# Kernel optimization log

Measured on AMD Instinct MI355X. Metric: run time of the kernel, lower is better.

Reference implementation:

```python
import jax, jax.numpy as jnp
import numpy as np

B, S, D, H = 2, 2048, 2048, 16
DH = D // H  # 128


def setup_inputs() -> dict:
    key = jax.random.key(0)
    ks = jax.random.split(key, 7)
    x = jax.random.normal(ks[0], (B, S, D), dtype=jnp.float32)
    # causal mask [b, s, s], True = attend
    mask = jnp.broadcast_to(jnp.tril(jnp.ones((S, S), dtype=bool)), (B, S, S))
    scale = 1.0 / np.sqrt(D)
    Wq = jax.random.normal(ks[1], (D, H, DH), dtype=jnp.float32) * scale
    Wk = jax.random.normal(ks[2], (D, 1, DH), dtype=jnp.float32) * scale
    Wv = jax.random.normal(ks[3], (D, 1, DH), dtype=jnp.float32) * scale
    Wo = jax.random.normal(ks[4], (H, DH, D), dtype=jnp.float32) * scale
    bo = jnp.zeros((D,), dtype=jnp.float32)
    return {"x": x, "mask": mask, "Wq": Wq, "Wk": Wk, "Wv": Wv, "Wo": Wo, "bo": bo}


def reference(x, mask, Wq, Wk, Wv, Wo, bo):
    # projections: q [b,s,h,dh]; k,v [b,s,1,dh] (single shared KV head)
    q = jnp.einsum("bsd,dhe->bshe", x, Wq)
    k = jnp.einsum("bsd,dhe->bshe", x, Wk)[:, :, 0, :]  # [b,s,dh]
    v = jnp.einsum("bsd,dhe->bshe", x, Wv)[:, :, 0, :]  # [b,s,dh]
    # scores [b,h,s,s] with 1/sqrt(d_head) scaling
    scores = jnp.einsum("bqhe,bke->bhqk", q, k) / jnp.sqrt(
        jnp.asarray(q.shape[-1], dtype=q.dtype)
    )
    big_neg = jnp.finfo(scores.dtype).min
    scores = jnp.where(mask[:, None, :, :], scores, big_neg)
    probs = jax.nn.softmax(scores, axis=-1)
    attn = jnp.einsum("bhqk,bke->bhqe", probs, v)  # [b,h,s,dh]
    # output projection contracting (head, d_head) -> d_state, with bias
    out = jnp.einsum("bhqe,hed->bqd", attn, Wo) + bo
    return out
```

## Files before the change

### kernel.cpp

```cpp
#include <hip/hip_runtime.h>
#include <cmath>
#include <cstdint>

typedef __bf16 bf16;
typedef __bf16 bf16x8 __attribute__((ext_vector_type(8)));
typedef __bf16 bf16x4 __attribute__((ext_vector_type(4)));
typedef float f32x4 __attribute__((ext_vector_type(4)));

#define SDIM 2048
#define DDIM 2048
#define NQKV 2304
#define DH   128

__device__ __forceinline__ void glds16(const bf16* g, bf16* l) {
    __builtin_amdgcn_global_load_lds(
        (const __attribute__((address_space(1))) void*)g,
        (__attribute__((address_space(3))) void*)l, 16, 0, 0);
}

#define MEMFENCE() asm volatile("" ::: "memory")
#define SBAR() do { MEMFENCE(); __builtin_amdgcn_s_barrier(); MEMFENCE(); } while (0)

__global__ __launch_bounds__(256) void prep_kernel(const float* __restrict__ x,
                                                   const float* __restrict__ Wq,
                                                   const float* __restrict__ Wk,
                                                   const float* __restrict__ Wv,
                                                   const float* __restrict__ Wo,
                                                   bf16* __restrict__ xb,
                                                   bf16* __restrict__ Wqkv_t,
                                                   bf16* __restrict__ Wo_t) {
    __shared__ float tile[32][33];
    int bx = blockIdx.x;
    if (bx < 8192) {
        int i = bx * 256 + threadIdx.x;
        float4 v = reinterpret_cast<const float4*>(x)[i];
        bf16x4 o;
        o[0] = (bf16)v.x; o[1] = (bf16)v.y; o[2] = (bf16)v.z; o[3] = (bf16)v.w;
        reinterpret_cast<bf16x4*>(xb)[i] = o;
        return;
    }
    bx -= 8192;
    const float* src; bf16* dst; int srcN; int t;
    if (bx < 4096)      { src = Wq; dst = Wqkv_t;                      srcN = 2048; t = bx; }
    else if (bx < 4352) { src = Wk; dst = Wqkv_t + (size_t)2048*2048;  srcN = 128;  t = bx - 4096; }
    else if (bx < 4608) { src = Wv; dst = Wqkv_t + (size_t)2176*2048;  srcN = 128;  t = bx - 4352; }
    else                { src = Wo; dst = Wo_t;                        srcN = 2048; t = bx - 4608; }
    const int srcK = 2048;
    int ntx = srcN >> 5;
    int n0 = (t % ntx) * 32, k0 = (t / ntx) * 32;
    int tx = threadIdx.x & 31;
    int ty = threadIdx.x >> 5;
    for (int i = 0; i < 4; i++)
        tile[ty + i*8][tx] = src[(size_t)(k0 + ty + i*8) * srcN + n0 + tx];
    __syncthreads();
    for (int i = 0; i < 4; i++)
        dst[(size_t)(n0 + ty + i*8) * srcK + k0 + tx] = (bf16)tile[tx][ty + i*8];
}

__global__ __launch_bounds__(256) void vtrans_kernel(const bf16* __restrict__ QKV,
                                                     bf16* __restrict__ Vt) {
    __shared__ bf16 tile[32][33];
    int tx = threadIdx.x & 31;
    int ty = threadIdx.x >> 5;
    int d0 = blockIdx.x * 32;
    int s0 = blockIdx.y * 32;
    int b  = blockIdx.z;
    for (int i = 0; i < 4; i++)
        tile[ty + i*8][tx] = QKV[((size_t)b * SDIM + s0 + ty + i*8) * NQKV + 2176 + d0 + tx];
    __syncthreads();
    for (int i = 0; i < 4; i++)
        Vt[((size_t)b * DH + d0 + ty + i*8) * SDIM + s0 + tx] = tile[tx][ty + i*8];
}

template<int WRITE_F32>
__global__ __launch_bounds__(512, 2) void gemm8_kernel(const bf16* __restrict__ A,
                                                       const bf16* __restrict__ Bt,
                                                       void* __restrict__ Cout,
                                                       const float* __restrict__ bias,
                                                       int N) {
    constexpr int K  = 2048;
    constexpr int NT = 32;
    __shared__ bf16 smem[65536];

    const int tid  = threadIdx.x;
    const int wave = tid >> 6, lane = tid & 63;
    const int quad = lane >> 4, l15 = lane & 15;
    const int wm = wave >> 2, wn = wave & 3;
    const int tm = blockIdx.x * 256, tn = blockIdx.y * 256;

    const int r0 = wave * 32 + (lane >> 2);
    const int cs = (lane & 3) ^ ((lane >> 3) & 3);
    const bf16* Ag = A  + (size_t)(tm + r0) * K + cs * 8;
    const bf16* Bg = Bt + (size_t)(tn + r0) * K + cs * 8;
    bf16* Asl = smem + wave * 1024;
    bf16* Bsl = smem + 32768 + wave * 1024;

    auto STAGE_A = [&](int t, int kh) {
        if (t < NT) {
            const bf16* s = Ag + t * 64 + kh * 32;
            bf16* d = Asl + (t & 1) * 16384 + kh * 8192;
            glds16(s, d);
            glds16(s + 16 * K, d + 512);
        }
    };
    auto STAGE_B = [&](int t, int kh) {
        if (t < NT) {
            const bf16* s = Bg + t * 64 + kh * 32;
            bf16* d = Bsl + (t & 1) * 16384 + kh * 8192;
            glds16(s, d);
            glds16(s + 16 * K, d + 512);
        }
    };

    const int rsw  = (l15 >> 1) & 3;
    const int aoff = (wm * 128 + l15) * 32 + ((quad ^ rsw) * 8);
    const int boff = (wn * 64  + l15) * 32 + ((quad ^ rsw) * 8);

    f32x4 acc[8][4];
#pragma unroll
    for (int m = 0; m < 8; m++)
#pragma unroll
        for (int n = 0; n < 4; n++) acc[m][n] = (f32x4)0.0f;

    STAGE_A(0, 0); STAGE_B(0, 0);
    STAGE_A(0, 1); STAGE_B(0, 1);
    STAGE_A(1, 0); STAGE_B(1, 0);
    asm volatile("s_waitcnt vmcnt(4)" ::: "memory");
    SBAR();

    bf16x8 av[4], bv[4];
    for (int t = 0; t < NT; ++t) {
        const int buf = t & 1;
        const bf16* Sa = smem + buf * 16384;
        const bf16* Sb = smem + 32768 + buf * 16384;

#pragma unroll
        for (int m = 0; m < 4; m++) av[m] = *reinterpret_cast<const bf16x8*>(Sa + aoff + m * 512);
#pragma unroll
        for (int n = 0; n < 4; n++) bv[n] = *reinterpret_cast<const bf16x8*>(Sb + boff + n * 512);
        STAGE_A(t + 1, 1);
        SBAR();
        __builtin_amdgcn_s_setprio(1);
#pragma unroll
        for (int m = 0; m < 4; m++)
#pragma unroll
            for (int n = 0; n < 4; n++)
                acc[m][n] = __builtin_amdgcn_mfma_f32_16x16x32_bf16(av[m], bv[n], acc[m][n], 0, 0, 0);
        __builtin_amdgcn_s_setprio(0);
        SBAR();

#pragma unroll
        for (int m = 0; m < 4; m++) av[m] = *reinterpret_cast<const bf16x8*>(Sa + aoff + 2048 + m * 512);
        STAGE_B(t + 1, 1);
        SBAR();
        __builtin_amdgcn_s_setprio(1);
#pragma unroll
        for (int m = 0; m < 4; m++)
#pragma unroll
            for (int n = 0; n < 4; n++)
                acc[4 + m][n] = __builtin_amdgcn_mfma_f32_16x16x32_bf16(av[m], bv[n], acc[4 + m][n], 0, 0, 0);
        __builtin_amdgcn_s_setprio(0);
        if (t + 1 < NT) { asm volatile("s_waitcnt vmcnt(8)" ::: "memory"); }
        else            { asm volatile("s_waitcnt vmcnt(0)" ::: "memory"); }
        SBAR();

#pragma unroll
        for (int m = 0; m < 4; m++) av[m] = *reinterpret_cast<const bf16x8*>(Sa + 8192 + aoff + m * 512);
#pragma unroll
        for (int n = 0; n < 4; n++) bv[n] = *reinterpret_cast<const bf16x8*>(Sb + 8192 + boff + n * 512);
        STAGE_A(t + 2, 0);
        SBAR();
        __builtin_amdgcn_s_setprio(1);
#pragma unroll
        for (int m = 0; m < 4; m++)
#pragma unroll
            for (int n = 0; n < 4; n++)
                acc[m][n] = __builtin_amdgcn_mfma_f32_16x16x32_bf16(av[m], bv[n], acc[m][n], 0, 0, 0);
        __builtin_amdgcn_s_setprio(0);
        SBAR();

#pragma unroll
        for (int m = 0; m < 4; m++) av[m] = *reinterpret_cast<const bf16x8*>(Sa + 8192 + aoff + 2048 + m * 512);
        STAGE_B(t + 2, 0);
        SBAR();
        __builtin_amdgcn_s_setprio(1);
#pragma unroll
        for (int m = 0; m < 4; m++)
#pragma unroll
            for (int n = 0; n < 4; n++)
                acc[4 + m][n] = __builtin_amdgcn_mfma_f32_16x16x32_bf16(av[m], bv[n], acc[4 + m][n], 0, 0, 0);
        __builtin_amdgcn_s_setprio(0);
        if (t + 2 < NT) { asm volatile("s_waitcnt vmcnt(4)" ::: "memory"); }
        else            { asm volatile("s_waitcnt vmcnt(0)" ::: "memory"); }
        SBAR();
    }

#pragma unroll
    for (int m = 0; m < 8; m++)
#pragma unroll
        for (int n = 0; n < 4; n++)
#pragma unroll
            for (int r = 0; r < 4; r++) {
                int row = tm + wm * 128 + m * 16 + quad * 4 + r;
                int col = tn + wn * 64 + n * 16 + l15;
                float v = acc[m][n][r];
                if (WRITE_F32)
                    reinterpret_cast<float*>(Cout)[(size_t)row * N + col] = v + bias[col];
                else
                    reinterpret_cast<bf16*>(Cout)[(size_t)row * N + col] = (bf16)v;
            }
}

#define FPLD 72

__global__ __launch_bounds__(512) void flash_kernel(const bf16* __restrict__ QKV,
                                                    const bf16* __restrict__ Vt,
                                                    bf16* __restrict__ attn) {
    __shared__ bf16 KVS[16384];
    __shared__ bf16 Ps[8 * 16 * FPLD];
    bf16* Ks  = KVS;
    bf16* Vts = KVS + 8192;

    const int tid  = threadIdx.x;
    const int wave = tid >> 6, lane = tid & 63;
    const int quad = lane >> 4, l15 = lane & 15;
    const int bx = blockIdx.x;
    const int qs = 255 - (bx >> 1);
    const int b  = bx & 1;
    const int q  = qs * 8 + wave;
    const size_t rowbase = (size_t)b * SDIM;
    const bf16* Vtb = Vt + (size_t)b * DH * SDIM;
    const float scale = 0.088388347648318447f;

    const int s0 = wave, s1 = wave + 8;
    const int krow0 = s0*4 + (lane >> 4), krow1 = s1*4 + (lane >> 4);
    const int kchunk = lane & 15;
    const bf16* kg0 = QKV + (rowbase + krow0) * NQKV + 2048 + ((kchunk ^ (krow0 & 15)) * 8);
    const bf16* kg1 = QKV + (rowbase + krow1) * NQKV + 2048 + ((kchunk ^ (krow1 & 15)) * 8);
    bf16* kl0 = Ks + s0 * 512;
    bf16* kl1 = Ks + s1 * 512;
    const int vrow0 = s0*8 + (lane >> 3), vrow1 = s1*8 + (lane >> 3);
    const int vchunk = lane & 7;
    const bf16* vg0 = Vtb + (size_t)vrow0 * SDIM + ((vchunk ^ (vrow0 & 7)) * 8);
    const bf16* vg1 = Vtb + (size_t)vrow1 * SDIM + ((vchunk ^ (vrow1 & 7)) * 8);
    bf16* vl0 = Vts + s0 * 512;
    bf16* vl1 = Vts + s1 * 512;

    bf16x8 qf[4];
    {
        const bf16* qp = QKV + (rowbase + q) * NQKV + l15 * DH + quad * 8;
        for (int kk = 0; kk < 4; kk++)
            qf[kk] = *reinterpret_cast<const bf16x8*>(qp + kk * 32);
    }
    float l_s[4] = {0.0f, 0.0f, 0.0f, 0.0f};
    f32x4 acc[8];
    for (int d = 0; d < 8; d++) acc[d] = (f32x4)0.0f;

    const int ntiles = (qs >> 3) + 1;
    bf16* Pw = Ps + wave * (16 * FPLD);

    const bf16* kp0 = kg0; const bf16* kp1 = kg1;
    const bf16* vp0 = vg0; const bf16* vp1 = vg1;

    for (int t = 0; t < ntiles; t++) {
        const int key0 = t * 64;
        __syncthreads();
        glds16(kp0, kl0); glds16(kp1, kl1);
        glds16(vp0, vl0); glds16(vp1, vl1);
        kp0 += 64 * NQKV; kp1 += 64 * NQKV; vp0 += 64; vp1 += 64;
        __syncthreads();

        f32x4 sc[4];
        for (int c = 0; c < 4; c++) sc[c] = (f32x4)0.0f;
        for (int c = 0; c < 4; c++)
            for (int kk = 0; kk < 4; kk++) {
                int j = (kk*4 + quad) ^ l15;
                bf16x8 kf = *reinterpret_cast<const bf16x8*>(
                    Ks + (c*16 + l15) * 128 + j * 8);
                sc[c] = __builtin_amdgcn_mfma_f32_16x16x32_bf16(qf[kk], kf, sc[c], 0, 0, 0);
            }

        const bool tail = (key0 + 63 > q);
        for (int c = 0; c < 4; c++)
            for (int r = 0; r < 4; r++) {
                float p;
                if (tail && (key0 + c*16 + l15 > q)) p = 0.0f;
                else p = __expf(sc[c][r] * scale);
                l_s[r] += p;
                Pw[(quad*4 + r) * FPLD + c*16 + l15] = (bf16)p;
            }

        for (int kk2 = 0; kk2 < 2; kk2++) {
            bf16x8 pf = *reinterpret_cast<const bf16x8*>(Pw + l15 * FPLD + kk2*32 + quad*8);
            for (int dd = 0; dd < 8; dd++) {
                int d = dd*16 + l15;
                int j = (kk2*4 + quad) ^ (l15 & 7);
                bf16x8 vf = *reinterpret_cast<const bf16x8*>(Vts + d * 64 + j * 8);
                acc[dd] = __builtin_amdgcn_mfma_f32_16x16x32_bf16(pf, vf, acc[dd], 0, 0, 0);
            }
        }
    }

    __syncthreads();

    for (int d = 1; d < 16; d <<= 1)
        for (int r = 0; r < 4; r++) l_s[r] += __shfl_xor(l_s[r], d);

    bf16* Ow = KVS + wave * 2048;
    for (int r = 0; r < 4; r++) {
        float inv = 1.0f / l_s[r];
        for (int d = 0; d < 8; d++)
            Ow[(quad*4 + r) * 128 + d*16 + l15] = (bf16)(acc[d][r] * inv);
    }
    const int orow = lane >> 2;
    const int ocol = (lane & 3) * 8;
    bf16* ob = attn + (rowbase + q) * (size_t)DDIM;
    for (int it = 0; it < 4; it++)
        *reinterpret_cast<uint4*>(ob + orow * DH + ocol + it*32) =
            *reinterpret_cast<const uint4*>(Ow + orow * 128 + ocol + it*32);
}

extern "C" void kernel_launch(void* const* d_in, const int* in_sizes, int n_in,
                              void* d_out, int out_size, void* d_ws, size_t ws_size,
                              hipStream_t stream) {
    const float* x  = (const float*)d_in[0];
    const float* Wq = (const float*)d_in[2];
    const float* Wk = (const float*)d_in[3];
    const float* Wv = (const float*)d_in[4];
    const float* Wo = (const float*)d_in[5];
    const float* bo = (const float*)d_in[6];
    float* out = (float*)d_out;

    char* ws = (char*)d_ws;
    bf16* xb     = (bf16*)(ws);
    bf16* Wqkv_t = (bf16*)(ws + 16777216);
    bf16* Wo_t   = (bf16*)(ws + 26214400);
    bf16* QKV    = (bf16*)(ws + 34603008);
    bf16* attn   = (bf16*)(ws + 53477376);
    bf16* Vtb    = (bf16*)(ws + 70254592);
    (void)ws_size; (void)in_sizes; (void)n_in; (void)out_size;

    prep_kernel<<<16896, 256, 0, stream>>>(x, Wq, Wk, Wv, Wo, xb, Wqkv_t, Wo_t);
    gemm8_kernel<0><<<dim3(16, 9), 512, 0, stream>>>(xb, Wqkv_t, (void*)QKV, nullptr, 2304);
    vtrans_kernel<<<dim3(4, 64, 2), 256, 0, stream>>>(QKV, Vtb);
    flash_kernel<<<512, 512, 0, stream>>>(QKV, Vtb, attn);
    gemm8_kernel<1><<<dim3(16, 8), 512, 0, stream>>>(attn, Wo_t, (void*)out, bo, 2048);
}
```

Measured before the change: 303.5 us.

## Double-buffer K/V tiles and keep P in registers in flash kernel

Rewrites the attention kernel so K/V tiles are prefetched into a second LDS buffer while the current tile is computed. Computing S^T (K as A operand) and permuting the V^T columns during the transpose lets P go straight from registers into the PV MFMA, so the LDS round trip for P disappears. Each block now has 4 waves, and each wave handles 2 query rows to reuse K/V fragments. Block scheduling is also reordered to pair long and short causal blocks. This removes barrier-bound load stalls and LDS traffic, at the cost of more registers and a doubled LDS footprint.

Measured after the change: 307.9 us. No clear change (+1.5%).

```diff
diff --git a/kernel.cpp b/kernel.cpp
--- a/kernel.cpp
+++ b/kernel.cpp
@@ -68,8 +68,10 @@
     for (int i = 0; i < 4; i++)
         tile[ty + i*8][tx] = QKV[((size_t)b * SDIM + s0 + ty + i*8) * NQKV + 2176 + d0 + tx];
     __syncthreads();
+    int pos = s0 + tx;
+    int pp = (pos & ~63) | (pos & 32) | ((pos & 12) << 1) | ((pos & 16) >> 2) | (pos & 3);
     for (int i = 0; i < 4; i++)
-        Vt[((size_t)b * DH + d0 + ty + i*8) * SDIM + s0 + tx] = tile[tx][ty + i*8];
+        Vt[((size_t)b * DH + d0 + ty + i*8) * SDIM + pp] = tile[tx][ty + i*8];
 }
 
 template<int WRITE_F32>
@@ -211,113 +213,156 @@
             }
 }
 
-#define FPLD 72
-
-__global__ __launch_bounds__(512) void flash_kernel(const bf16* __restrict__ QKV,
+__global__ __launch_bounds__(256) void flash_kernel(const bf16* __restrict__ QKV,
                                                     const bf16* __restrict__ Vt,
                                                     bf16* __restrict__ attn) {
-    __shared__ bf16 KVS[16384];
-    __shared__ bf16 Ps[8 * 16 * FPLD];
-    bf16* Ks  = KVS;
-    bf16* Vts = KVS + 8192;
-
+    __shared__ __align__(16) bf16 KVS[32768];
     const int tid  = threadIdx.x;
     const int wave = tid >> 6, lane = tid & 63;
     const int quad = lane >> 4, l15 = lane & 15;
     const int bx = blockIdx.x;
-    const int qs = 255 - (bx >> 1);
-    const int b  = bx & 1;
-    const int q  = qs * 8 + wave;
+    const int u  = (bx < 256) ? bx : bx - 256;
+    const int qs = (bx < 256) ? (255 - (u >> 1)) : (u >> 1);
+    const int b  = u & 1;
+    const int q0 = qs * 8 + wave * 2;
     const size_t rowbase = (size_t)b * SDIM;
     const bf16* Vtb = Vt + (size_t)b * DH * SDIM;
     const float scale = 0.088388347648318447f;
 
-    const int s0 = wave, s1 = wave + 8;
-    const int krow0 = s0*4 + (lane >> 4), krow1 = s1*4 + (lane >> 4);
-    const int kchunk = lane & 15;
-    const bf16* kg0 = QKV + (rowbase + krow0) * NQKV + 2048 + ((kchunk ^ (krow0 & 15)) * 8);
-    const bf16* kg1 = QKV + (rowbase + krow1) * NQKV + 2048 + ((kchunk ^ (krow1 & 15)) * 8);
-    bf16* kl0 = Ks + s0 * 512;
-    bf16* kl1 = Ks + s1 * 512;
-    const int vrow0 = s0*8 + (lane >> 3), vrow1 = s1*8 + (lane >> 3);
-    const int vchunk = lane & 7;
-    const bf16* vg0 = Vtb + (size_t)vrow0 * SDIM + ((vchunk ^ (vrow0 & 7)) * 8);
-    const bf16* vg1 = Vtb + (size_t)vrow1 * SDIM + ((vchunk ^ (vrow1 & 7)) * 8);
-    bf16* vl0 = Vts + s0 * 512;
-    bf16* vl1 = Vts + s1 * 512;
-
-    bf16x8 qf[4];
-    {
-        const bf16* qp = QKV + (rowbase + q) * NQKV + l15 * DH + quad * 8;
-        for (int kk = 0; kk < 4; kk++)
-            qf[kk] = *reinterpret_cast<const bf16x8*>(qp + kk * 32);
-    }
-    float l_s[4] = {0.0f, 0.0f, 0.0f, 0.0f};
-    f32x4 acc[8];
-    for (int d = 0; d < 8; d++) acc[d] = (f32x4)0.0f;
+    const bf16* kgp[4]; const bf16* vgp[4];
+#pragma unroll
+    for (int i = 0; i < 4; i++) {
+        int s = wave * 4 + i;
+        int krow = s * 4 + (lane >> 4);
+        kgp[i] = QKV + (rowbase + krow) * NQKV + 2048 + (((lane & 15) ^ (krow & 15)) * 8);
+        int vrow = s * 8 + (lane >> 3);
+        vgp[i] = Vtb + (size_t)vrow * SDIM + (((lane & 7) ^ (vrow & 7)) * 8);
+    }
+
+    bf16x8 qf[2][4];
+#pragma unroll
+    for (int r2 = 0; r2 < 2; r2++) {
+        const bf16* qp = QKV + (rowbase + q0 + r2) * NQKV + l15 * DH + quad * 8;
+#pragma unroll
+        for (int kk = 0; kk < 4; kk++) qf[r2][kk] = *reinterpret_cast<const bf16x8*>(qp + kk * 32);
+    }
+
+    f32x4 acc[2][8];
+#pragma unroll
+    for (int r2 = 0; r2 < 2; r2++)
+#pragma unroll
+        for (int d = 0; d < 8; d++) acc[r2][d] = (f32x4)0.0f;
+    float l_s[2] = {0.0f, 0.0f};
 
     const int ntiles = (qs >> 3) + 1;
-    bf16* Pw = Ps + wave * (16 * FPLD);
-
-    const bf16* kp0 = kg0; const bf16* kp1 = kg1;
-    const bf16* vp0 = vg0; const bf16* vp1 = vg1;
+
+#pragma unroll
+    for (int i = 0; i < 4; i++) {
+        glds16(kgp[i], KVS + (wave*4 + i) * 512);
+        glds16(vgp[i], KVS + 8192 + (wave*4 + i) * 512);
+        kgp[i] += 64 * NQKV; vgp[i] += 64;
+    }
 
     for (int t = 0; t < ntiles; t++) {
+        if (t + 1 < ntiles) {
+            const int bo = ((t + 1) & 1) << 14;
+#pragma unroll
+            for (int i = 0; i < 4; i++) {
+                glds16(kgp[i], KVS + bo + (wave*4 + i) * 512);
+                glds16(vgp[i], KVS + bo + 8192 + (wave*4 + i) * 512);
+                kgp[i] += 64 * NQKV; vgp[i] += 64;
+            }
+            asm volatile("s_waitcnt vmcnt(8)" ::: "memory");
+        } else {
+            asm volatile("s_waitcnt vmcnt(0)" ::: "memory");
+        }
+        SBAR();
+        const bf16* Ks  = KVS + ((t & 1) << 14);
+        const bf16* Vts = Ks + 8192;
         const int key0 = t * 64;
-        __syncthreads();
-        glds16(kp0, kl0); glds16(kp1, kl1);
-        glds16(vp0, vl0); glds16(vp1, vl1);
-        kp0 += 64 * NQKV; kp1 += 64 * NQKV; vp0 += 64; vp1 += 64;
-        __syncthreads();
-
-        f32x4 sc[4];
-        for (int c = 0; c < 4; c++) sc[c] = (f32x4)0.0f;
+
+        f32x4 sc[2][4];
+#pragma unroll
+        for (int r2 = 0; r2 < 2; r2++)
+#pragma unroll
+            for (int c = 0; c < 4; c++) sc[r2][c] = (f32x4)0.0f;
+        __builtin_amdgcn_s_setprio(1);
+#pragma unroll
         for (int c = 0; c < 4; c++)
+#pragma unroll
             for (int kk = 0; kk < 4; kk++) {
-                int j = (kk*4 + quad) ^ l15;
                 bf16x8 kf = *reinterpret_cast<const bf16x8*>(
-                    Ks + (c*16 + l15) * 128 + j * 8);
-                sc[c] = __builtin_amdgcn_mfma_f32_16x16x32_bf16(qf[kk], kf, sc[c], 0, 0, 0);
+                    Ks + (c*16 + l15) * 128 + (((kk*4 + quad) ^ l15) * 8));
+                sc[0][c] = __builtin_amdgcn_mfma_f32_16x16x32_bf16(kf, qf[0][kk], sc[0][c], 0, 0, 0);
+                sc[1][c] = __builtin_amdgcn_mfma_f32_16x16x32_bf16(kf, qf[1][kk], sc[1][c], 0, 0, 0);
             }
-
-        const bool tail = (key0 + 63 > q);
-        for (int c = 0; c < 4; c++)
-            for (int r = 0; r < 4; r++) {
-                float p;
-                if (tail && (key0 + c*16 + l15 > q)) p = 0.0f;
-                else p = __expf(sc[c][r] * scale);
-                l_s[r] += p;
-                Pw[(quad*4 + r) * FPLD + c*16 + l15] = (bf16)p;
+        __builtin_amdgcn_s_setprio(0);
+
+        bf16x8 pa[2][2];
+#pragma unroll
+        for (int r2 = 0; r2 < 2; r2++) {
+            const int q = q0 + r2;
+            const bool tail = (key0 + 63 > q);
+            float ps = 0.0f;
+#pragma unroll
+            for (int c = 0; c < 4; c++)
+#pragma unroll
+                for (int r = 0; r < 4; r++) {
+                    int key = key0 + c*16 + quad*4 + r;
+                    float pv = (tail && key > q) ? 0.0f : __expf(sc[r2][c][r] * scale);
+                    ps += pv;
+                    pa[r2][c >> 1][(c & 1)*4 + r] = (bf16)pv;
+                }
+            l_s[r2] += ps;
+        }
+
+        __builtin_amdgcn_s_setprio(1);
+#pragma unroll
+        for (int kk2 = 0; kk2 < 2; kk2++)
+#pragma unroll
+            for (int dd = 0; dd < 8; dd++) {
+                bf16x8 vf = *reinterpret_cast<const bf16x8*>(
+                    Vts + (dd*16 + l15) * 64 + (((kk2*4 + quad) ^ (l15 & 7)) * 8));
+                acc[0][dd] = __builtin_amdgcn_mfma_f32_16x16x32_bf16(pa[0][kk2], vf, acc[0][dd], 0, 0, 0);
+                acc[1][dd] = __builtin_amdgcn_mfma_f32_16x16x32_bf16(pa[1][kk2], vf, acc[1][dd], 0, 0, 0);
             }
-
-        for (int kk2 = 0; kk2 < 2; kk2++) {
-            bf16x8 pf = *reinterpret_cast<const bf16x8*>(Pw + l15 * FPLD + kk2*32 + quad*8);
-            for (int dd = 0; dd < 8; dd++) {
-                int d = dd*16 + l15;
-                int j = (kk2*4 + quad) ^ (l15 & 7);
-                bf16x8 vf = *reinterpret_cast<const bf16x8*>(Vts + d * 64 + j * 8);
-                acc[dd] = __builtin_amdgcn_mfma_f32_16x16x32_bf16(pf, vf, acc[dd], 0, 0, 0);
-            }
-        }
+        __builtin_amdgcn_s_setprio(0);
+        SBAR();
     }
 
     __syncthreads();
 
-    for (int d = 1; d < 16; d <<= 1)
-        for (int r = 0; r < 4; r++) l_s[r] += __shfl_xor(l_s[r], d);
-
-    bf16* Ow = KVS + wave * 2048;
-    for (int r = 0; r < 4; r++) {
-        float inv = 1.0f / l_s[r];
-        for (int d = 0; d < 8; d++)
-            Ow[(quad*4 + r) * 128 + d*16 + l15] = (bf16)(acc[d][r] * inv);
-    }
+    float linv[2];
+#pragma unroll
+    for (int r2 = 0; r2 < 2; r2++) {
+        float v = l_s[r2];
+        v += __shfl_xor(v, 16);
+        v += __shfl_xor(v, 32);
+        linv[r2] = 1.0f / v;
+    }
+
+    bf16* Ow = KVS + wave * 4096;
+#pragma unroll
+    for (int r2 = 0; r2 < 2; r2++)
+#pragma unroll
+        for (int r = 0; r < 4; r++) {
+            float inv = __shfl(linv[r2], quad*4 + r);
+#pragma unroll
+            for (int dd = 0; dd < 8; dd++)
+                Ow[r2*2048 + (quad*4 + r)*128 + dd*16 + l15] = (bf16)(acc[r2][dd][r] * inv);
+        }
+    __syncthreads();
     const int orow = lane >> 2;
     const int ocol = (lane & 3) * 8;
-    bf16* ob = attn + (rowbase + q) * (size_t)DDIM;
-    for (int it = 0; it < 4; it++)
-        *reinterpret_cast<uint4*>(ob + orow * DH + ocol + it*32) =
-            *reinterpret_cast<const uint4*>(Ow + orow * 128 + ocol + it*32);
+#pragma unroll
+    for (int rr = 0; rr < 2; rr++) {
+        bf16* ob = attn + (rowbase + q0 + rr) * (size_t)DDIM;
+        const bf16* Os = KVS + wave * 4096 + rr * 2048;
+#pragma unroll
+        for (int it = 0; it < 4; it++)
+            *reinterpret_cast<uint4*>(ob + orow * DH + ocol + it*32) =
+                *reinterpret_cast<const uint4*>(Os + orow * 128 + ocol + it*32);
+    }
 }
 
 extern "C" void kernel_launch(void* const* d_in, const int* in_sizes, int n_in,
@@ -343,6 +388,6 @@
     prep_kernel<<<16896, 256, 0, stream>>>(x, Wq, Wk, Wv, Wo, xb, Wqkv_t, Wo_t);
     gemm8_kernel<0><<<dim3(16, 9), 512, 0, stream>>>(xb, Wqkv_t, (void*)QKV, nullptr, 2304);
     vtrans_kernel<<<dim3(4, 64, 2), 256, 0, stream>>>(QKV, Vtb);
-    flash_kernel<<<512, 512, 0, stream>>>(QKV, Vtb, attn);
+    flash_kernel<<<512, 256, 0, stream>>>(QKV, Vtb, attn);
     gemm8_kernel<1><<<dim3(16, 8), 512, 0, stream>>>(attn, Wo_t, (void*)out, bo, 2048);
 }
```
